# Kernel tuning notes

Measured on AMD Instinct MI355X. Metric: run time of the kernel, lower is better.

## Reference

```python
import jax, jax.numpy as jnp
import numpy as np

N_ITERS = 1000  # hardcoded in the original module
EPS = 1e-6


def setup_inputs() -> dict:
    key = jax.random.key(0)
    k1, k2 = jax.random.split(key)
    embeds = jax.random.normal(k1, (30000, 64), dtype=jnp.float32)
    # torch does t.rand(...) inside forward; we hoist it here for determinism
    init_centroids = jax.random.uniform(k2, (500, 64), dtype=jnp.float32)
    return {"embeds": embeds, "init_centroids": init_centroids}


def reference(embeds, init_centroids):
    N, D = embeds.shape
    K = init_centroids.shape[0]
    # ||e||^2 is loop-invariant; squared L2 distance expanded as
    # ||e||^2 - 2 e.c + ||c||^2 (same math as (e-c)^2.sum(-1), no [N,K,D] blowup)
    e_sq = jnp.sum(embeds * embeds, axis=1)  # [N]
    ones = jnp.ones((N, 1), dtype=embeds.dtype)

    def step(carry, _):
        cents, _, _ = carry
        c_sq = jnp.sum(cents * cents, axis=1)  # [K]
        dists = e_sq[:, None] - 2.0 * (embeds @ cents.T) + c_sq[None, :]  # [N,K]
        idxs = jnp.argmin(dists, axis=1)  # [N] int32
        sums = jax.ops.segment_sum(embeds, idxs, num_segments=K)  # [K,D]
        counts = jax.ops.segment_sum(ones, idxs, num_segments=K)  # [K,1]
        new_cents = sums / (counts + EPS)
        return (new_cents, idxs, counts), None

    init = (init_centroids,
            jnp.zeros((N,), dtype=jnp.int32),
            jnp.zeros((K, 1), dtype=embeds.dtype))
    (centroids, idxs, clust_nums), _ = jax.lax.scan(step, init, None, length=N_ITERS)
    return centroids, idxs, clust_nums
```

## Files before the change

kernel.cpp:

```cpp
#include <hip/hip_runtime.h>
#include <math.h>

#define N_PTS   30000
#define DIM     64
#define K_C     500
#define K_PAD   512
#define N_ITERS 1000

#define TM    128
#define NTM   235
#define GRID  NTM
#define BLK   512

#define FPSCALE 262144.0f
#define INV_FPSCALE (1.0 / 262144.0)

#define BAR_STRIDE 32
#define BAR_REL_OFF (GRID * BAR_STRIDE)

__device__ __forceinline__ int SLOT(int i) { return (i / 12) * K_PAD + 500 + (i % 12); }
#define MLS(i)  SLOT(i)
#define CNT_ML  SLOT(128)

__device__ __forceinline__ void gridbar(int* bar, int n) {
  __syncthreads();
  if (blockIdx.x == 0) {
    const int t = threadIdx.x;
    if (t >= 1 && t < GRID) {
      while (__hip_atomic_load(&bar[t * BAR_STRIDE], __ATOMIC_RELAXED,
                               __HIP_MEMORY_SCOPE_AGENT) < n)
        __builtin_amdgcn_s_sleep(2);
      __builtin_amdgcn_fence(__ATOMIC_ACQUIRE, "agent");
    }
    __syncthreads();
    if (t == 0)
      __hip_atomic_store(&bar[BAR_REL_OFF], n, __ATOMIC_RELEASE,
                         __HIP_MEMORY_SCOPE_AGENT);
  } else {
    if (threadIdx.x == 0) {
      __hip_atomic_store(&bar[blockIdx.x * BAR_STRIDE], n, __ATOMIC_RELEASE,
                         __HIP_MEMORY_SCOPE_AGENT);
      while (__hip_atomic_load(&bar[BAR_REL_OFF], __ATOMIC_RELAXED,
                               __HIP_MEMORY_SCOPE_AGENT) < n)
        __builtin_amdgcn_s_sleep(2);
      __builtin_amdgcn_fence(__ATOMIC_ACQUIRE, "agent");
    }
    __syncthreads();
  }
}

__global__ __launch_bounds__(BLK)
void k_persist(const float* __restrict__ embeds,
               const float* __restrict__ cents0,
               float* __restrict__ esq,
               int* __restrict__ idx,
               int* __restrict__ gcnt,
               unsigned long long* __restrict__ acc,
               int* mov,
               float* __restrict__ csq_g,
               int* __restrict__ changed,
               int* __restrict__ bar,
               float* __restrict__ out) {
  __shared__ __align__(16) float As[DIM * TM];
  __shared__ __align__(16) float Bs[DIM * K_PAD];
  int* BsI = (int*)Bs;
  const int tid = threadIdx.x;
  const int bid = blockIdx.x;
  int bno = 0;

  {
    const int w = bid * 8 + (tid >> 6), d = tid & 63;
    for (int p = w; p < N_PTS; p += GRID * 8) {
      float v = embeds[(size_t)p * DIM + d];
      float s = v * v;
      #pragma unroll
      for (int m = 1; m < 64; m <<= 1) s += __shfl_xor(s, m, 64);
      if (d == 0) esq[p] = s;
    }
  }
  gridbar(bar, ++bno);

  const int m0 = bid * TM;
  const int tx = tid & 31, ty = tid >> 5;

  #pragma unroll
  for (int l = 0; l < 4; ++l) {
    int e = tid + l * BLK;
    int pl = e & 127, d4 = e >> 7;
    int p = m0 + pl;
    float4 v = make_float4(0.f, 0.f, 0.f, 0.f);
    if (p < N_PTS) v = *reinterpret_cast<const float4*>(embeds + (size_t)p * DIM + d4 * 4);
    As[(d4 * 4 + 0) * TM + pl] = v.x; As[(d4 * 4 + 1) * TM + pl] = v.y;
    As[(d4 * 4 + 2) * TM + pl] = v.z; As[(d4 * 4 + 3) * TM + pl] = v.w;
  }

  for (int it = 0; it < N_ITERS; ++it) {
    if (tid == 0) BsI[CNT_ML] = 0;

    {
      bool doStage;
      if (it == 0)      doStage = true;
      else if (it == 1) doStage = (tid < K_C);
      else              doStage = (tid < K_C) && (mov[tid] >= it - 1);
      if (doStage) {
        float s4[16];
        if (it == 0) {
          if (tid < K_C) {
            #pragma unroll
            for (int l = 0; l < 16; ++l) {
              float4 v = *reinterpret_cast<const float4*>(cents0 + (size_t)tid * DIM + l * 4);
              Bs[(l * 4 + 0) * K_PAD + tid] = v.x; Bs[(l * 4 + 1) * K_PAD + tid] = v.y;
              Bs[(l * 4 + 2) * K_PAD + tid] = v.z; Bs[(l * 4 + 3) * K_PAD + tid] = v.w;
              s4[l] = (v.x * v.x + v.y * v.y) + (v.z * v.z + v.w * v.w);
            }
          } else {
            #pragma unroll
            for (int l = 0; l < 16; ++l) {
              Bs[(l * 4 + 0) * K_PAD + tid] = 0.f; Bs[(l * 4 + 1) * K_PAD + tid] = 0.f;
              Bs[(l * 4 + 2) * K_PAD + tid] = 0.f; Bs[(l * 4 + 3) * K_PAD + tid] = 0.f;
              s4[l] = 0.f;
            }
          }
        } else {
          float fc = (float)gcnt[tid] + 1e-6f;
          #pragma unroll
          for (int l = 0; l < 16; ++l) {
            const unsigned long long* ap = acc + (size_t)tid * DIM + l * 4;
            longlong2 a0 = *reinterpret_cast<const longlong2*>(ap);
            longlong2 a1 = *reinterpret_cast<const longlong2*>(ap + 2);
            float n0 = (float)((double)a0.x * INV_FPSCALE) / fc;
            float n1 = (float)((double)a0.y * INV_FPSCALE) / fc;
            float n2 = (float)((double)a1.x * INV_FPSCALE) / fc;
            float n3 = (float)((double)a1.y * INV_FPSCALE) / fc;
            Bs[(l * 4 + 0) * K_PAD + tid] = n0; Bs[(l * 4 + 1) * K_PAD + tid] = n1;
            Bs[(l * 4 + 2) * K_PAD + tid] = n2; Bs[(l * 4 + 3) * K_PAD + tid] = n3;
            s4[l] = (n0 * n0 + n1 * n1) + (n2 * n2 + n3 * n3);
          }
        }
        float s8[8], s16[4], s32[2];
        #pragma unroll
        for (int m = 0; m < 8; ++m) s8[m] = s4[2 * m] + s4[2 * m + 1];
        #pragma unroll
        for (int m = 0; m < 4; ++m) s16[m] = s8[2 * m] + s8[2 * m + 1];
        s32[0] = s16[0] + s16[1]; s32[1] = s16[2] + s16[3];
        float cs = s32[0] + s32[1];
        csq_g[tid] = (tid < K_C) ? cs : INFINITY;
      }
    }
    __syncthreads();

    float best[8]; int bidx[8];
    #pragma unroll
    for (int i = 0; i < 8; ++i) { best[i] = INFINITY; bidx[i] = 0; }

    #pragma unroll
    for (int h = 0; h < 2; ++h) {
      const float* ap = As + ty * 8;
      const float* bp = Bs + h * 256 + tx * 4;

      float acc_r[8][8];
      #pragma unroll
      for (int i = 0; i < 8; ++i)
        #pragma unroll
        for (int j = 0; j < 8; ++j) acc_r[i][j] = 0.f;

      float4 a0 = *reinterpret_cast<const float4*>(ap);
      float4 a1 = *reinterpret_cast<const float4*>(ap + 4);
      float4 b0 = *reinterpret_cast<const float4*>(bp);
      float4 b1 = *reinterpret_cast<const float4*>(bp + 128);

      #pragma unroll 8
      for (int d = 0; d < DIM; ++d) {
        const int dn = (d + 1 < DIM) ? d + 1 : d;
        float4 na0 = *reinterpret_cast<const float4*>(ap + dn * TM);
        float4 na1 = *reinterpret_cast<const float4*>(ap + dn * TM + 4);
        float4 nb0 = *reinterpret_cast<const float4*>(bp + dn * K_PAD);
        float4 nb1 = *reinterpret_cast<const float4*>(bp + dn * K_PAD + 128);

        float av[8] = {a0.x, a0.y, a0.z, a0.w, a1.x, a1.y, a1.z, a1.w};
        float bv[8] = {b0.x, b0.y, b0.z, b0.w, b1.x, b1.y, b1.z, b1.w};
        #pragma unroll
        for (int i = 0; i < 8; ++i)
          #pragma unroll
          for (int j = 0; j < 8; ++j)
            acc_r[i][j] = fmaf(av[i], bv[j], acc_r[i][j]);

        a0 = na0; a1 = na1; b0 = nb0; b1 = nb1;
      }

      float esq_h[8];
      #pragma unroll
      for (int i = 0; i < 8; ++i) {
        int p = m0 + ty * 8 + i;
        esq_h[i] = (p < N_PTS) ? esq[p] : 0.f;
      }
      const int nbase = h * 256;
      float4 c0 = *reinterpret_cast<const float4*>(csq_g + nbase + tx * 4);
      float4 c1 = *reinterpret_cast<const float4*>(csq_g + nbase + 128 + tx * 4);
      float cv[8] = {c0.x, c0.y, c0.z, c0.w, c1.x, c1.y, c1.z, c1.w};
      #pragma unroll
      for (int g = 0; g < 2; ++g) {
        #pragma unroll
        for (int j = 0; j < 4; ++j) {
          int c = g * 4 + j;
          int n = nbase + g * 128 + tx * 4 + j;
          #pragma unroll
          for (int i = 0; i < 8; ++i) {
            float dd = (esq_h[i] - 2.0f * acc_r[i][c]) + cv[c];
            if (dd < best[i]) { best[i] = dd; bidx[i] = n; }
          }
        }
      }
    }

    #pragma unroll
    for (int i = 0; i < 8; ++i) {
      float v = best[i]; int bi = bidx[i];
      #pragma unroll
      for (int s = 1; s < 32; s <<= 1) {
        float ov = __shfl_xor(v, s, 64);
        int   oi = __shfl_xor(bi, s, 64);
        if (ov < v || (ov == v && oi < bi)) { v = ov; bi = oi; }
      }
      if (tx == 0) {
        int pl = ty * 8 + i, p = m0 + pl;
        if (p < N_PTS) {
          int old = idx[p];
          if (old != bi) {
            idx[p] = bi;
            int slot = atomicAdd(&BsI[CNT_ML], 1);
            BsI[MLS(slot)] = pl | ((old + 1) << 7) | (bi << 16);
            if (slot == 0)
              __hip_atomic_store(&changed[it], 1, __ATOMIC_RELAXED,
                                 __HIP_MEMORY_SCOPE_AGENT);
          }
        }
      }
    }
    __syncthreads();

    {
      const int w8 = tid >> 6, lane = tid & 63;
      const int cnt = BsI[CNT_ML];
      for (int i = w8; i < cnt; i += 8) {
        int e = BsI[MLS(i)];
        int pl = e & 127, old = ((e >> 7) & 511) - 1, k = e >> 16;
        float v = embeds[(size_t)(m0 + pl) * DIM + lane];
        long long iv = (long long)__float2int_rn(v * FPSCALE);
        atomicAdd(&acc[(size_t)k * DIM + lane], (unsigned long long)iv);
        if (old >= 0)
          atomicAdd(&acc[(size_t)old * DIM + lane], (unsigned long long)(-iv));
        if (lane == 0) {
          atomicAdd(&gcnt[k], 1);
          __hip_atomic_store(&mov[k], it, __ATOMIC_RELAXED, __HIP_MEMORY_SCOPE_AGENT);
          if (old >= 0) {
            atomicAdd(&gcnt[old], -1);
            __hip_atomic_store(&mov[old], it, __ATOMIC_RELAXED, __HIP_MEMORY_SCOPE_AGENT);
          }
        }
      }
    }
    gridbar(bar, ++bno);

    if (__hip_atomic_load(&changed[it], __ATOMIC_RELAXED,
                          __HIP_MEMORY_SCOPE_AGENT) == 0)
      break;
  }

  const int tot = K_C * DIM + N_PTS + K_C;
  for (int g = bid * BLK + tid; g < tot; g += GRID * BLK) {
    float v;
    if (g < K_C * DIM) {
      int k = g >> 6;
      v = (float)((double)(long long)acc[g] * INV_FPSCALE) / ((float)gcnt[k] + 1e-6f);
    } else if (g < K_C * DIM + N_PTS) {
      v = (float)idx[g - K_C * DIM];
    } else {
      v = (float)gcnt[g - K_C * DIM - N_PTS];
    }
    out[g] = v;
  }
}

extern "C" void kernel_launch(void* const* d_in, const int* in_sizes, int n_in,
                              void* d_out, int out_size, void* d_ws, size_t ws_size,
                              hipStream_t stream) {
  const float* embeds = (const float*)d_in[0];
  const float* init_c = (const float*)d_in[1];
  float* out = (float*)d_out;

  char* w = (char*)d_ws;
  size_t off = 0;
  auto alloc = [&](size_t bytes) -> void* {
    void* p = w + off;
    off += (bytes + 255) & ~(size_t)255;
    return p;
  };
  float* cents0 = (float*)alloc((size_t)K_C * DIM * sizeof(float));
  float* esq    = (float*)alloc((size_t)N_PTS * sizeof(float));
  int*   idx    = (int*)  alloc((size_t)N_PTS * sizeof(int));
  int*   gcnt   = (int*)  alloc((size_t)K_C * sizeof(int));
  unsigned long long* acc =
      (unsigned long long*)alloc((size_t)K_C * DIM * sizeof(unsigned long long));
  int*   mov    = (int*)  alloc((size_t)K_PAD * sizeof(int));
  float* csq_g  = (float*)alloc((size_t)K_PAD * sizeof(float));
  int*   chg    = (int*)  alloc((size_t)N_ITERS * sizeof(int));
  int*   bar    = (int*)  alloc((size_t)(BAR_REL_OFF + 64) * sizeof(int));

  hipMemcpyAsync(cents0, init_c, (size_t)K_C * DIM * sizeof(float),
                 hipMemcpyDeviceToDevice, stream);
  hipMemsetAsync(gcnt, 0, (size_t)K_C * sizeof(int), stream);
  hipMemsetAsync(acc, 0, (size_t)K_C * DIM * sizeof(unsigned long long), stream);
  hipMemsetAsync(idx, 0xFF, (size_t)N_PTS * sizeof(int), stream);
  hipMemsetAsync(mov, 0xFF, (size_t)K_PAD * sizeof(int), stream);
  hipMemsetAsync(chg, 0, (size_t)N_ITERS * sizeof(int), stream);
  hipMemsetAsync(bar, 0, (size_t)(BAR_REL_OFF + 64) * sizeof(int), stream);

  k_persist<<<dim3(GRID), dim3(BLK), 0, stream>>>(
      embeds, cents0, esq, idx, gcnt, acc, mov, csq_g, chg, bar, out);
}
```

Before: 1.903 ms.

## Move point tile to global memory with wave-uniform loads and 16x2 register tiling

Removes the shared-memory copy of the block's point tile and writes a transposed copy to a global workspace. The distance GEMM is retiled so each wave owns 16 points and each lane covers 2 centroids. Point loads then use a wave-uniform address via readfirstlane, so they can become scalar loads through the scalar cache. Squared norms are hoisted into registers once, outside the iteration loop. This cuts LDS traffic and frees LDS, but relies on scalar-cache hits for the A operand each iteration and adds a 64-lane argmin shuffle instead of 32.

```diff
diff --git a/kernel.cpp b/kernel.cpp
--- a/kernel.cpp
+++ b/kernel.cpp
@@ -53,6 +53,7 @@
 void k_persist(const float* __restrict__ embeds,
                const float* __restrict__ cents0,
                float* __restrict__ esq,
+               float* __restrict__ aT_g,
                int* __restrict__ idx,
                int* __restrict__ gcnt,
                unsigned long long* __restrict__ acc,
@@ -61,11 +62,11 @@
                int* __restrict__ changed,
                int* __restrict__ bar,
                float* __restrict__ out) {
-  __shared__ __align__(16) float As[DIM * TM];
   __shared__ __align__(16) float Bs[DIM * K_PAD];
   int* BsI = (int*)Bs;
   const int tid = threadIdx.x;
   const int bid = blockIdx.x;
+  const int m0 = bid * TM;
   int bno = 0;
 
   {
@@ -78,11 +79,7 @@
       if (d == 0) esq[p] = s;
     }
   }
-  gridbar(bar, ++bno);
-
-  const int m0 = bid * TM;
-  const int tx = tid & 31, ty = tid >> 5;
-
+  float* aT = aT_g + (size_t)bid * (DIM * TM);
   #pragma unroll
   for (int l = 0; l < 4; ++l) {
     int e = tid + l * BLK;
@@ -90,8 +87,20 @@
     int p = m0 + pl;
     float4 v = make_float4(0.f, 0.f, 0.f, 0.f);
     if (p < N_PTS) v = *reinterpret_cast<const float4*>(embeds + (size_t)p * DIM + d4 * 4);
-    As[(d4 * 4 + 0) * TM + pl] = v.x; As[(d4 * 4 + 1) * TM + pl] = v.y;
-    As[(d4 * 4 + 2) * TM + pl] = v.z; As[(d4 * 4 + 3) * TM + pl] = v.w;
+    aT[(d4 * 4 + 0) * TM + pl] = v.x; aT[(d4 * 4 + 1) * TM + pl] = v.y;
+    aT[(d4 * 4 + 2) * TM + pl] = v.z; aT[(d4 * 4 + 3) * TM + pl] = v.w;
+  }
+  gridbar(bar, ++bno);
+
+  const int tx = tid & 63;
+  const int tyw = __builtin_amdgcn_readfirstlane(tid >> 6);
+  const float* aTr = aT + tyw * 16;
+
+  float esq_r[16];
+  #pragma unroll
+  for (int i = 0; i < 16; ++i) {
+    int p = m0 + tyw * 16 + i;
+    esq_r[i] = (p < N_PTS) ? esq[p] : 0.f;
   }
 
   for (int it = 0; it < N_ITERS; ++it) {
@@ -149,81 +158,63 @@
     }
     __syncthreads();
 
-    float best[8]; int bidx[8];
+    float best[16]; int bidx[16];
     #pragma unroll
-    for (int i = 0; i < 8; ++i) { best[i] = INFINITY; bidx[i] = 0; }
+    for (int i = 0; i < 16; ++i) { best[i] = INFINITY; bidx[i] = 0; }
 
     #pragma unroll
-    for (int h = 0; h < 2; ++h) {
-      const float* ap = As + ty * 8;
-      const float* bp = Bs + h * 256 + tx * 4;
-
-      float acc_r[8][8];
+    for (int h = 0; h < 4; ++h) {
+      const float* bp = Bs + h * 128 + tx * 2;
+      float accr[16][2];
       #pragma unroll
-      for (int i = 0; i < 8; ++i)
-        #pragma unroll
-        for (int j = 0; j < 8; ++j) acc_r[i][j] = 0.f;
-
-      float4 a0 = *reinterpret_cast<const float4*>(ap);
-      float4 a1 = *reinterpret_cast<const float4*>(ap + 4);
-      float4 b0 = *reinterpret_cast<const float4*>(bp);
-      float4 b1 = *reinterpret_cast<const float4*>(bp + 128);
-
-      #pragma unroll 8
+      for (int i = 0; i < 16; ++i) { accr[i][0] = 0.f; accr[i][1] = 0.f; }
+
+      float2 b = *reinterpret_cast<const float2*>(bp);
+      const float* ad = aTr;
+      #pragma unroll 16
       for (int d = 0; d < DIM; ++d) {
         const int dn = (d + 1 < DIM) ? d + 1 : d;
-        float4 na0 = *reinterpret_cast<const float4*>(ap + dn * TM);
-        float4 na1 = *reinterpret_cast<const float4*>(ap + dn * TM + 4);
-        float4 nb0 = *reinterpret_cast<const float4*>(bp + dn * K_PAD);
-        float4 nb1 = *reinterpret_cast<const float4*>(bp + dn * K_PAD + 128);
-
-        float av[8] = {a0.x, a0.y, a0.z, a0.w, a1.x, a1.y, a1.z, a1.w};
-        float bv[8] = {b0.x, b0.y, b0.z, b0.w, b1.x, b1.y, b1.z, b1.w};
+        float2 nb = *reinterpret_cast<const float2*>(bp + dn * K_PAD);
+        float4 s0 = *reinterpret_cast<const float4*>(ad);
+        float4 s1 = *reinterpret_cast<const float4*>(ad + 4);
+        float4 s2 = *reinterpret_cast<const float4*>(ad + 8);
+        float4 s3 = *reinterpret_cast<const float4*>(ad + 12);
+        float av[16] = {s0.x, s0.y, s0.z, s0.w, s1.x, s1.y, s1.z, s1.w,
+                        s2.x, s2.y, s2.z, s2.w, s3.x, s3.y, s3.z, s3.w};
         #pragma unroll
-        for (int i = 0; i < 8; ++i)
-          #pragma unroll
-          for (int j = 0; j < 8; ++j)
-            acc_r[i][j] = fmaf(av[i], bv[j], acc_r[i][j]);
-
-        a0 = na0; a1 = na1; b0 = nb0; b1 = nb1;
-      }
-
-      float esq_h[8];
+        for (int i = 0; i < 16; ++i) {
+          accr[i][0] = fmaf(av[i], b.x, accr[i][0]);
+          accr[i][1] = fmaf(av[i], b.y, accr[i][1]);
+        }
+        b = nb;
+        ad += TM;
+      }
+
+      const int nbase = h * 128;
+      float2 cq = *reinterpret_cast<const float2*>(csq_g + nbase + tx * 2);
       #pragma unroll
-      for (int i = 0; i < 8; ++i) {
-        int p = m0 + ty * 8 + i;
-        esq_h[i] = (p < N_PTS) ? esq[p] : 0.f;
-      }
-      const int nbase = h * 256;
-      float4 c0 = *reinterpret_cast<const float4*>(csq_g + nbase + tx * 4);
-      float4 c1 = *reinterpret_cast<const float4*>(csq_g + nbase + 128 + tx * 4);
-      float cv[8] = {c0.x, c0.y, c0.z, c0.w, c1.x, c1.y, c1.z, c1.w};
-      #pragma unroll
-      for (int g = 0; g < 2; ++g) {
+      for (int j = 0; j < 2; ++j) {
+        float cj = (j == 0) ? cq.x : cq.y;
+        int n = nbase + tx * 2 + j;
         #pragma unroll
-        for (int j = 0; j < 4; ++j) {
-          int c = g * 4 + j;
-          int n = nbase + g * 128 + tx * 4 + j;
-          #pragma unroll
-          for (int i = 0; i < 8; ++i) {
-            float dd = (esq_h[i] - 2.0f * acc_r[i][c]) + cv[c];
-            if (dd < best[i]) { best[i] = dd; bidx[i] = n; }
-          }
+        for (int i = 0; i < 16; ++i) {
+          float dd = (esq_r[i] - 2.0f * accr[i][j]) + cj;
+          if (dd < best[i]) { best[i] = dd; bidx[i] = n; }
         }
       }
     }
 
     #pragma unroll
-    for (int i = 0; i < 8; ++i) {
+    for (int i = 0; i < 16; ++i) {
       float v = best[i]; int bi = bidx[i];
       #pragma unroll
-      for (int s = 1; s < 32; s <<= 1) {
+      for (int s = 1; s < 64; s <<= 1) {
         float ov = __shfl_xor(v, s, 64);
         int   oi = __shfl_xor(bi, s, 64);
         if (ov < v || (ov == v && oi < bi)) { v = ov; bi = oi; }
       }
       if (tx == 0) {
-        int pl = ty * 8 + i, p = m0 + pl;
+        int pl = tyw * 16 + i, p = m0 + pl;
         if (p < N_PTS) {
           int old = idx[p];
           if (old != bi) {
@@ -298,6 +289,7 @@
   };
   float* cents0 = (float*)alloc((size_t)K_C * DIM * sizeof(float));
   float* esq    = (float*)alloc((size_t)N_PTS * sizeof(float));
+  float* aT_g   = (float*)alloc((size_t)NTM * DIM * TM * sizeof(float));
   int*   idx    = (int*)  alloc((size_t)N_PTS * sizeof(int));
   int*   gcnt   = (int*)  alloc((size_t)K_C * sizeof(int));
   unsigned long long* acc =
@@ -317,5 +309,5 @@
   hipMemsetAsync(bar, 0, (size_t)(BAR_REL_OFF + 64) * sizeof(int), stream);
 
   k_persist<<<dim3(GRID), dim3(BLK), 0, stream>>>(
-      embeds, cents0, esq, idx, gcnt, acc, mov, csq_g, chg, bar, out);
+      embeds, cents0, esq, aT_g, idx, gcnt, acc, mov, csq_g, chg, bar, out);
 }
```

Result: slower. 3.737 ms (+96.4%).
